# Optimization experiments

Hardware: AMD Instinct MI355X
Metric: run time of the kernel (lower is better)

Reference implementation:

```python
import jax, jax.numpy as jnp
import numpy as np

N = 50000   # nodes
E = 800000  # edges
H = 64      # hidden channels
EPS = 1e-16  # PyG softmax denominator epsilon


def _ptconv(x, pos, src, dst, W_src, W_dst, W_val, W_pos, b_pos):
    """PyG PointTransformerConv: per-edge gather, positional MLP, vector
    attention (segment softmax over edges grouped by dst), scatter-sum.
    edge_index convention: src = j (neighbor), dst = i (center)."""
    a_src = x @ W_src          # [N,H] alpha_j projection
    a_dst = x @ W_dst          # [N,H] alpha_i projection
    v = x @ W_val              # [N,H] values
    # relative positional encoding: pos_nn(pos_i - pos_j), [E,H]
    delta = (pos[dst] - pos[src]) @ W_pos + b_pos
    alpha = a_dst[dst] - a_src[src] + delta           # [E,H]
    # numerically-stable vector softmax over variable-size neighborhoods
    m = jax.lax.stop_gradient(jax.ops.segment_max(alpha, dst, num_segments=N))
    e = jnp.exp(alpha - m[dst])
    s = jax.ops.segment_sum(e, dst, num_segments=N)
    attn = e / (s[dst] + EPS)                         # [E,H]
    return jax.ops.segment_sum(attn * (v[src] + delta), dst, num_segments=N)


def setup_inputs() -> dict:
    key = jax.random.key(0)
    ks = jax.random.split(key, 16)
    x = jax.random.normal(ks[0], (N, 3), dtype=jnp.float32)
    pos = jax.random.normal(ks[1], (N, 3), dtype=jnp.float32)
    edge_index = jax.random.randint(ks[2], (2, E), 0, N)
    batch = jnp.zeros((N,), dtype=jnp.int32)

    def lin(k, i, o):
        return (jax.random.normal(k, (i, o), dtype=jnp.float32)
                * np.float32(1.0 / np.sqrt(i)))

    return {
        "x": x, "pos": pos, "edge_index": edge_index, "batch": batch,
        # conv1 (in=3 -> H)
        "W1_src": lin(ks[3], 3, H), "W1_dst": lin(ks[4], 3, H),
        "W1_val": lin(ks[5], 3, H),
        "W1_pos": lin(ks[6], 3, H), "b1_pos": jnp.zeros((H,), jnp.float32),
        # conv2 (H -> H)
        "W2_src": lin(ks[7], H, H), "W2_dst": lin(ks[8], H, H),
        "W2_val": lin(ks[9], H, H),
        "W2_pos": lin(ks[10], 3, H), "b2_pos": jnp.zeros((H,), jnp.float32),
        # MLP head
        "W_fc1": lin(ks[11], H, H // 2), "b_fc1": jnp.zeros((H // 2,), jnp.float32),
        "W_fc2": lin(ks[12], H // 2, 1), "b_fc2": jnp.zeros((1,), jnp.float32),
    }


def reference(x, pos, edge_index, batch,
              W1_src, W1_dst, W1_val, W1_pos, b1_pos,
              W2_src, W2_dst, W2_val, W2_pos, b2_pos,
              W_fc1, b_fc1, W_fc2, b_fc2):
    src, dst = edge_index[0], edge_index[1]
    h = jax.nn.relu(_ptconv(x, pos, src, dst, W1_src, W1_dst, W1_val, W1_pos, b1_pos))
    h = jax.nn.relu(_ptconv(h, pos, src, dst, W2_src, W2_dst, W2_val, W2_pos, b2_pos))
    h = jax.nn.relu(h @ W_fc1 + b_fc1)
    return h @ W_fc2 + b_fc2  # [N, 1]
```

## Files before the change

### kernel.cpp

```cpp
#include <hip/hip_runtime.h>
#include <hip/hip_fp16.h>
#include <math.h>


#define LOG2E 1.44269504088896340736f

typedef _Float16 hf2 __attribute__((ext_vector_type(2)));
union H2U { __half2 hh; hf2 hf; unsigned u; };
union WPack { uint2 u2; struct { unsigned s, v; } w; };

#if defined(__has_builtin)
#if __has_builtin(__builtin_amdgcn_fdot2)
#define HAVE_FDOT2 1
#endif
#endif

__device__ __forceinline__ float fdot2(hf2 a, hf2 b, float c) {
#ifdef HAVE_FDOT2
    return __builtin_amdgcn_fdot2(a, b, c, false);
#else
    return fmaf((float)a.x, (float)b.x, fmaf((float)a.y, (float)b.y, c));
#endif
}

__global__ void __launch_bounds__(256) hist_proj1_kernel(
        const int* __restrict__ dst, int* __restrict__ count, int* __restrict__ rank,
        const float* __restrict__ x, const float* __restrict__ pos,
        const float* __restrict__ W1_src, const float* __restrict__ W1_val,
        const float* __restrict__ W1_pos,
        __half2* __restrict__ g1, int N, int E) {
    int gtid = blockIdx.x * 256 + threadIdx.x;
    int gsz = gridDim.x * 256;
    for (int e = gtid; e < E; e += gsz)
        rank[e] = atomicAdd(&count[dst[e]], 1);
    for (int t = gtid; t < N * 64; t += gsz) {
        int node = t >> 6, c = t & 63;
        float x0 = x[node * 3 + 0], x1 = x[node * 3 + 1], x2 = x[node * 3 + 2];
        float p0 = pos[node * 3 + 0], p1 = pos[node * 3 + 1], p2 = pos[node * 3 + 2];
        float as = fmaf(x0, W1_src[c], fmaf(x1, W1_src[64 + c], x2 * W1_src[128 + c]));
        float vv = fmaf(x0, W1_val[c], fmaf(x1, W1_val[64 + c], x2 * W1_val[128 + c]));
        float cc = fmaf(p0, W1_pos[c], fmaf(p1, W1_pos[64 + c], p2 * W1_pos[128 + c]));
        g1[t] = __floats2half2_rn((as + cc) * LOG2E, vv - cc);
    }
}

__global__ void __launch_bounds__(256) scan_kernel(
        const int* __restrict__ count, int* __restrict__ offsets, int n, int nsb) {
    __shared__ int red[4];
    __shared__ int wpre[4];
    int tid = threadIdx.x, lane = tid & 63, wid = tid >> 6;
    int lim = blockIdx.x * 1024;
    int s = 0;
    for (int i = tid * 4; i < lim; i += 1024) {
        int4 c = *(const int4*)&count[i];
        s += c.x + c.y + c.z + c.w;
    }
    #pragma unroll
    for (int off = 32; off >= 1; off >>= 1) s += __shfl_down(s, off);
    if (lane == 0) red[wid] = s;
    __syncthreads();
    int base = red[0] + red[1] + red[2] + red[3];

    int b4 = lim + tid * 4;
    int4 c = make_int4(0, 0, 0, 0);
    if (b4 + 3 < n) {
        c = *(const int4*)&count[b4];
    } else {
        if (b4 + 0 < n) c.x = count[b4 + 0];
        if (b4 + 1 < n) c.y = count[b4 + 1];
        if (b4 + 2 < n) c.z = count[b4 + 2];
    }
    int tsum = c.x + c.y + c.z + c.w;
    int inc = tsum;
    #pragma unroll
    for (int off = 1; off < 64; off <<= 1) {
        int t2 = __shfl_up(inc, off);
        if (lane >= off) inc += t2;
    }
    if (lane == 63) wpre[wid] = inc;
    __syncthreads();
    int wbase = 0;
    for (int q = 0; q < wid; ++q) wbase += wpre[q];
    int excl = base + wbase + (inc - tsum);
    if (b4 + 0 < n) offsets[b4 + 0] = excl;
    if (b4 + 1 < n) offsets[b4 + 1] = excl + c.x;
    if (b4 + 2 < n) offsets[b4 + 2] = excl + c.x + c.y;
    if (b4 + 3 < n) offsets[b4 + 3] = excl + c.x + c.y + c.z;
    if ((int)blockIdx.x == nsb - 1 && tid == 0)
        offsets[n] = base + wpre[0] + wpre[1] + wpre[2] + wpre[3];
}

__global__ void __launch_bounds__(256) scatter_kernel(
        const int* __restrict__ src, const int* __restrict__ dst,
        const int* __restrict__ rank, const int* __restrict__ offsets,
        int* __restrict__ sorted_src, int E) {
    int e = blockIdx.x * 256 + threadIdx.x;
    if (e < E) sorted_src[offsets[dst[e]] + rank[e]] = src[e];
}

__device__ __forceinline__ void eacc(float d2, __half2 gh, float& s, float& nvv) {
    float ax = __low2float(gh);
    float vv = __high2float(gh);
    float ev = exp2f(d2 - ax);
    s += ev;
    nvv = fmaf(ev, vv, nvv);
}

__device__ __forceinline__ float edge_node(
        int node, int laneoff,
        const int* __restrict__ offsets, const int* __restrict__ ss,
        const char* __restrict__ gbase, float d2, float dv) {
    int beg = offsets[node], end = offsets[node + 1];
    float s0 = 0.f, n0 = 0.f, s1 = 0.f, n1 = 0.f;
    int e = beg;
    int aligned = min((beg + 3) & ~3, end);
    for (; e < aligned; ++e) {
        int i0 = __builtin_amdgcn_readfirstlane(ss[e]);
        __half2 g0 = *(const __half2*)(gbase + (((size_t)(unsigned)i0) << 8) + laneoff);
        eacc(d2, g0, s0, n0);
    }
    for (; e + 8 <= end; e += 8) {
        int4 ia = *(const int4*)(ss + e);
        int4 ib = *(const int4*)(ss + e + 4);
        int i0 = __builtin_amdgcn_readfirstlane(ia.x);
        int i1 = __builtin_amdgcn_readfirstlane(ia.y);
        int i2 = __builtin_amdgcn_readfirstlane(ia.z);
        int i3 = __builtin_amdgcn_readfirstlane(ia.w);
        int i4 = __builtin_amdgcn_readfirstlane(ib.x);
        int i5 = __builtin_amdgcn_readfirstlane(ib.y);
        int i6 = __builtin_amdgcn_readfirstlane(ib.z);
        int i7 = __builtin_amdgcn_readfirstlane(ib.w);
        __half2 g0 = *(const __half2*)(gbase + (((size_t)(unsigned)i0) << 8) + laneoff);
        __half2 g1 = *(const __half2*)(gbase + (((size_t)(unsigned)i1) << 8) + laneoff);
        __half2 g2 = *(const __half2*)(gbase + (((size_t)(unsigned)i2) << 8) + laneoff);
        __half2 g3 = *(const __half2*)(gbase + (((size_t)(unsigned)i3) << 8) + laneoff);
        __half2 g4 = *(const __half2*)(gbase + (((size_t)(unsigned)i4) << 8) + laneoff);
        __half2 g5 = *(const __half2*)(gbase + (((size_t)(unsigned)i5) << 8) + laneoff);
        __half2 g6 = *(const __half2*)(gbase + (((size_t)(unsigned)i6) << 8) + laneoff);
        __half2 g7 = *(const __half2*)(gbase + (((size_t)(unsigned)i7) << 8) + laneoff);
        eacc(d2, g0, s0, n0);
        eacc(d2, g1, s1, n1);
        eacc(d2, g2, s0, n0);
        eacc(d2, g3, s1, n1);
        eacc(d2, g4, s0, n0);
        eacc(d2, g5, s1, n1);
        eacc(d2, g6, s0, n0);
        eacc(d2, g7, s1, n1);
    }
    for (; e + 4 <= end; e += 4) {
        int4 ia = *(const int4*)(ss + e);
        int i0 = __builtin_amdgcn_readfirstlane(ia.x);
        int i1 = __builtin_amdgcn_readfirstlane(ia.y);
        int i2 = __builtin_amdgcn_readfirstlane(ia.z);
        int i3 = __builtin_amdgcn_readfirstlane(ia.w);
        __half2 g0 = *(const __half2*)(gbase + (((size_t)(unsigned)i0) << 8) + laneoff);
        __half2 g1 = *(const __half2*)(gbase + (((size_t)(unsigned)i1) << 8) + laneoff);
        __half2 g2 = *(const __half2*)(gbase + (((size_t)(unsigned)i2) << 8) + laneoff);
        __half2 g3 = *(const __half2*)(gbase + (((size_t)(unsigned)i3) << 8) + laneoff);
        eacc(d2, g0, s0, n0);
        eacc(d2, g1, s1, n1);
        eacc(d2, g2, s0, n0);
        eacc(d2, g3, s1, n1);
    }
    for (; e < end; ++e) {
        int i0 = __builtin_amdgcn_readfirstlane(ss[e]);
        __half2 g0 = *(const __half2*)(gbase + (((size_t)(unsigned)i0) << 8) + laneoff);
        eacc(d2, g0, s0, n0);
    }
    float s = s0 + s1;
    float num = fmaf(dv, s, n0 + n1);
    return fmaxf(num / (s + 1e-16f), 0.f);
}

__global__ void __launch_bounds__(256, 8) e1p2_kernel(
        const float* __restrict__ pos,
        const int* __restrict__ offsets, const int* __restrict__ sorted_src,
        const __half2* __restrict__ g1,
        const float* __restrict__ W1_pos, const float* __restrict__ b1_pos,
        const float* __restrict__ W2_src, const float* __restrict__ W2_val,
        const float* __restrict__ W2_pos,
        __half2* __restrict__ g2, int N) {
    __shared__ uint2 W4[2048];
    __shared__ __half hsh[4][64];
    int tid = threadIdx.x, lane = tid & 63, wid = tid >> 6;
    for (int idx = tid; idx < 2048; idx += 256) {
        int kk = idx >> 6, c = idx & 63;
        H2U ws, wv;
        ws.hh = __floats2half2_rn(W2_src[(2 * kk) * 64 + c], W2_src[(2 * kk + 1) * 64 + c]);
        wv.hh = __floats2half2_rn(W2_val[(2 * kk) * 64 + c], W2_val[(2 * kk + 1) * 64 + c]);
        W4[idx] = make_uint2(ws.u, wv.u);
    }
    __syncthreads();

    float w1p0 = W1_pos[lane], w1p1 = W1_pos[64 + lane], w1p2 = W1_pos[128 + lane];
    float bp1 = b1_pos[lane];
    float w2p0 = W2_pos[lane], w2p1 = W2_pos[64 + lane], w2p2 = W2_pos[128 + lane];
    int laneoff = lane * 4;
    int nwav = gridDim.x * 4;

    for (int node = blockIdx.x * 4 + wid; node < N; node += nwav) {
        float p0 = pos[node * 3 + 0], p1 = pos[node * 3 + 1], p2 = pos[node * 3 + 2];
        float dpos = fmaf(p0, w1p0, fmaf(p1, w1p1, p2 * w1p2));
        float hval = edge_node(node, laneoff, offsets, sorted_src,
                               (const char*)g1, dpos * LOG2E, dpos + bp1);
        hsh[wid][lane] = __float2half(hval);
        const hf2* h2 = (const hf2*)hsh[wid];
        float as = 0.f, vv = 0.f;
        #pragma unroll 8
        for (int kk = 0; kk < 32; ++kk) {
            hf2 hk = h2[kk];
            WPack wp; wp.u2 = W4[kk * 64 + lane];
            H2U a, b; a.u = wp.w.s; b.u = wp.w.v;
            as = fdot2(hk, a.hf, as);
            vv = fdot2(hk, b.hf, vv);
        }
        float cc = fmaf(p0, w2p0, fmaf(p1, w2p1, p2 * w2p2));
        g2[node * 64 + lane] = __floats2half2_rn((as + cc) * LOG2E, vv - cc);
    }
}

__global__ void __launch_bounds__(256, 8) e2head_kernel(
        const float* __restrict__ pos,
        const int* __restrict__ offsets, const int* __restrict__ sorted_src,
        const __half2* __restrict__ g2,
        const float* __restrict__ W2_pos, const float* __restrict__ b2_pos,
        const float* __restrict__ Wfc1, const float* __restrict__ bfc1,
        const float* __restrict__ Wfc2, const float* __restrict__ bfc2,
        float* __restrict__ out, int N) {
    __shared__ unsigned Wf2[1024];
    __shared__ __half hsh[4][64];
    int tid = threadIdx.x, lane = tid & 63, wid = tid >> 6;
    for (int idx = tid; idx < 1024; idx += 256) {
        int kk = idx >> 5, c = idx & 31;
        H2U w;
        w.hh = __floats2half2_rn(Wfc1[(2 * kk) * 32 + c], Wfc1[(2 * kk + 1) * 32 + c]);
        Wf2[idx] = w.u;
    }
    __syncthreads();

    float wp0 = W2_pos[lane], wp1 = W2_pos[64 + lane], wp2 = W2_pos[128 + lane];
    float bp = b2_pos[lane];
    int c = lane & 31, khb = (lane >> 5) * 16;
    float bfc1c = bfc1[c], wfc2c = Wfc2[c], bias2 = bfc2[0];
    int laneoff = lane * 4;
    int nwav = gridDim.x * 4;

    for (int node = blockIdx.x * 4 + wid; node < N; node += nwav) {
        float p0 = pos[node * 3 + 0], p1 = pos[node * 3 + 1], p2 = pos[node * 3 + 2];
        float dpos = fmaf(p0, wp0, fmaf(p1, wp1, p2 * wp2));
        float hval = edge_node(node, laneoff, offsets, sorted_src,
                               (const char*)g2, dpos * LOG2E, dpos + bp);
        hsh[wid][lane] = __float2half(hval);
        const hf2* h2 = (const hf2*)hsh[wid];
        float t2 = 0.f;
        #pragma unroll 8
        for (int j = 0; j < 16; ++j) {
            hf2 hk = h2[khb + j];
            H2U w; w.u = Wf2[(khb + j) * 32 + c];
            t2 = fdot2(hk, w.hf, t2);
        }
        t2 += __shfl_down(t2, 32);
        t2 = fmaxf(t2 + bfc1c, 0.f) * wfc2c;
        t2 = (lane < 32) ? t2 : 0.f;
        #pragma unroll
        for (int off = 16; off >= 1; off >>= 1) t2 += __shfl_down(t2, off);
        if (lane == 0) out[node] = t2 + bias2;
    }
}

extern "C" void kernel_launch(void* const* d_in, const int* in_sizes, int n_in,
                              void* d_out, int out_size, void* d_ws, size_t ws_size,
                              hipStream_t stream) {
    const float* x   = (const float*)d_in[0];
    const float* pos = (const float*)d_in[1];
    const int* eidx  = (const int*)d_in[2];
    const float* W1_src = (const float*)d_in[4];
    const float* W1_val = (const float*)d_in[6];
    const float* W1_pos = (const float*)d_in[7];
    const float* b1_pos = (const float*)d_in[8];
    const float* W2_src = (const float*)d_in[9];
    const float* W2_val = (const float*)d_in[11];
    const float* W2_pos = (const float*)d_in[12];
    const float* b2_pos = (const float*)d_in[13];
    const float* W_fc1  = (const float*)d_in[14];
    const float* b_fc1  = (const float*)d_in[15];
    const float* W_fc2  = (const float*)d_in[16];
    const float* b_fc2  = (const float*)d_in[17];

    const int N = in_sizes[0] / 3;
    const int E = in_sizes[2] / 2;
    const int* src = eidx;
    const int* dst = eidx + E;
    const int nsb = (N + 1023) / 1024;

    char* w = (char*)d_ws;
    auto carve = [&](size_t bytes) -> void* {
        void* p = (void*)w;
        w += (bytes + 255) & ~size_t(255);
        return p;
    };
    int*     count      = (int*)carve((size_t)N * 4);
    int*     offsets    = (int*)carve((size_t)(N + 1) * 4);
    int*     rank       = (int*)carve((size_t)E * 4);
    int*     sorted_src = (int*)carve((size_t)E * 4);
    __half2* g1         = (__half2*)carve((size_t)N * 64 * 4);
    __half2* g2         = (__half2*)carve((size_t)N * 64 * 4);

    hipMemsetAsync(count, 0, (size_t)N * 4, stream);
    hist_proj1_kernel<<<(N * 64 + 255) / 256, 256, 0, stream>>>(
        dst, count, rank, x, pos, W1_src, W1_val, W1_pos, g1, N, E);
    scan_kernel<<<nsb, 256, 0, stream>>>(count, offsets, N, nsb);
    scatter_kernel<<<(E + 255) / 256, 256, 0, stream>>>(src, dst, rank, offsets,
                                                        sorted_src, E);
    e1p2_kernel<<<2048, 256, 0, stream>>>(
        pos, offsets, sorted_src, g1, W1_pos, b1_pos, W2_src, W2_val, W2_pos, g2, N);
    e2head_kernel<<<2048, 256, 0, stream>>>(
        pos, offsets, sorted_src, g2, W2_pos, b2_pos,
        W_fc1, b_fc1, W_fc2, b_fc2, (float*)d_out, N);
}
```

Before: 246.4 us.

## Factor softmax exponent per source node and gather precomputed fp32 exp payloads

Measured after the change: 269.8 us. 1.09x slower.

```diff
diff --git a/kernel.cpp b/kernel.cpp
--- a/kernel.cpp
+++ b/kernel.cpp
@@ -7,7 +7,6 @@
 
 typedef _Float16 hf2 __attribute__((ext_vector_type(2)));
 union H2U { __half2 hh; hf2 hf; unsigned u; };
-union WPack { uint2 u2; struct { unsigned s, v; } w; };
 
 #if defined(__has_builtin)
 #if __has_builtin(__builtin_amdgcn_fdot2)
@@ -23,24 +22,35 @@
 #endif
 }
 
+__device__ __forceinline__ float2 pack_payload(float a_plus_c, float vv) {
+    float t = fminf(fmaxf(-a_plus_c * LOG2E, -86.6f), 86.6f);
+    float E = exp2f(t);
+    return make_float2(E, E * vv);
+}
+
 __global__ void __launch_bounds__(256) hist_proj1_kernel(
         const int* __restrict__ dst, int* __restrict__ count, int* __restrict__ rank,
         const float* __restrict__ x, const float* __restrict__ pos,
         const float* __restrict__ W1_src, const float* __restrict__ W1_val,
         const float* __restrict__ W1_pos,
-        __half2* __restrict__ g1, int N, int E) {
+        float2* __restrict__ g1, int N, int E) {
     int gtid = blockIdx.x * 256 + threadIdx.x;
     int gsz = gridDim.x * 256;
     for (int e = gtid; e < E; e += gsz)
         rank[e] = atomicAdd(&count[dst[e]], 1);
-    for (int t = gtid; t < N * 64; t += gsz) {
-        int node = t >> 6, c = t & 63;
+
+    int lane = threadIdx.x & 63, wid = threadIdx.x >> 6;
+    float ws0 = W1_src[lane], ws1 = W1_src[64 + lane], ws2 = W1_src[128 + lane];
+    float wv0 = W1_val[lane], wv1 = W1_val[64 + lane], wv2 = W1_val[128 + lane];
+    float wp0 = W1_pos[lane], wp1 = W1_pos[64 + lane], wp2 = W1_pos[128 + lane];
+    int nwav = gridDim.x * 4;
+    for (int node = blockIdx.x * 4 + wid; node < N; node += nwav) {
         float x0 = x[node * 3 + 0], x1 = x[node * 3 + 1], x2 = x[node * 3 + 2];
         float p0 = pos[node * 3 + 0], p1 = pos[node * 3 + 1], p2 = pos[node * 3 + 2];
-        float as = fmaf(x0, W1_src[c], fmaf(x1, W1_src[64 + c], x2 * W1_src[128 + c]));
-        float vv = fmaf(x0, W1_val[c], fmaf(x1, W1_val[64 + c], x2 * W1_val[128 + c]));
-        float cc = fmaf(p0, W1_pos[c], fmaf(p1, W1_pos[64 + c], p2 * W1_pos[128 + c]));
-        g1[t] = __floats2half2_rn((as + cc) * LOG2E, vv - cc);
+        float as = fmaf(x0, ws0, fmaf(x1, ws1, x2 * ws2));
+        float vv = fmaf(x0, wv0, fmaf(x1, wv1, x2 * wv2));
+        float cc = fmaf(p0, wp0, fmaf(p1, wp1, p2 * wp2));
+        g1[node * 64 + lane] = pack_payload(as + cc, vv - cc);
     }
 }
 
@@ -98,26 +108,19 @@
     if (e < E) sorted_src[offsets[dst[e]] + rank[e]] = src[e];
 }
 
-__device__ __forceinline__ void eacc(float d2, __half2 gh, float& s, float& nvv) {
-    float ax = __low2float(gh);
-    float vv = __high2float(gh);
-    float ev = exp2f(d2 - ax);
-    s += ev;
-    nvv = fmaf(ev, vv, nvv);
-}
-
 __device__ __forceinline__ float edge_node(
         int node, int laneoff,
         const int* __restrict__ offsets, const int* __restrict__ ss,
-        const char* __restrict__ gbase, float d2, float dv) {
+        const char* __restrict__ gbase, float dv) {
     int beg = offsets[node], end = offsets[node + 1];
+    if (beg >= end) return 0.f;
     float s0 = 0.f, n0 = 0.f, s1 = 0.f, n1 = 0.f;
     int e = beg;
     int aligned = min((beg + 3) & ~3, end);
     for (; e < aligned; ++e) {
         int i0 = __builtin_amdgcn_readfirstlane(ss[e]);
-        __half2 g0 = *(const __half2*)(gbase + (((size_t)(unsigned)i0) << 8) + laneoff);
-        eacc(d2, g0, s0, n0);
+        float2 g0 = *(const float2*)(gbase + (((size_t)(unsigned)i0) << 9) + laneoff);
+        s0 += g0.x; n0 += g0.y;
     }
     for (; e + 8 <= end; e += 8) {
         int4 ia = *(const int4*)(ss + e);
@@ -130,22 +133,22 @@
         int i5 = __builtin_amdgcn_readfirstlane(ib.y);
         int i6 = __builtin_amdgcn_readfirstlane(ib.z);
         int i7 = __builtin_amdgcn_readfirstlane(ib.w);
-        __half2 g0 = *(const __half2*)(gbase + (((size_t)(unsigned)i0) << 8) + laneoff);
-        __half2 g1 = *(const __half2*)(gbase + (((size_t)(unsigned)i1) << 8) + laneoff);
-        __half2 g2 = *(const __half2*)(gbase + (((size_t)(unsigned)i2) << 8) + laneoff);
-        __half2 g3 = *(const __half2*)(gbase + (((size_t)(unsigned)i3) << 8) + laneoff);
-        __half2 g4 = *(const __half2*)(gbase + (((size_t)(unsigned)i4) << 8) + laneoff);
-        __half2 g5 = *(const __half2*)(gbase + (((size_t)(unsigned)i5) << 8) + laneoff);
-        __half2 g6 = *(const __half2*)(gbase + (((size_t)(unsigned)i6) << 8) + laneoff);
-        __half2 g7 = *(const __half2*)(gbase + (((size_t)(unsigned)i7) << 8) + laneoff);
-        eacc(d2, g0, s0, n0);
-        eacc(d2, g1, s1, n1);
-        eacc(d2, g2, s0, n0);
-        eacc(d2, g3, s1, n1);
-        eacc(d2, g4, s0, n0);
-        eacc(d2, g5, s1, n1);
-        eacc(d2, g6, s0, n0);
-        eacc(d2, g7, s1, n1);
+        float2 g0 = *(const float2*)(gbase + (((size_t)(unsigned)i0) << 9) + laneoff);
+        float2 g1 = *(const float2*)(gbase + (((size_t)(unsigned)i1) << 9) + laneoff);
+        float2 g2 = *(const float2*)(gbase + (((size_t)(unsigned)i2) << 9) + laneoff);
+        float2 g3 = *(const float2*)(gbase + (((size_t)(unsigned)i3) << 9) + laneoff);
+        float2 g4 = *(const float2*)(gbase + (((size_t)(unsigned)i4) << 9) + laneoff);
+        float2 g5 = *(const float2*)(gbase + (((size_t)(unsigned)i5) << 9) + laneoff);
+        float2 g6 = *(const float2*)(gbase + (((size_t)(unsigned)i6) << 9) + laneoff);
+        float2 g7 = *(const float2*)(gbase + (((size_t)(unsigned)i7) << 9) + laneoff);
+        s0 += g0.x; n0 += g0.y;
+        s1 += g1.x; n1 += g1.y;
+        s0 += g2.x; n0 += g2.y;
+        s1 += g3.x; n1 += g3.y;
+        s0 += g4.x; n0 += g4.y;
+        s1 += g5.x; n1 += g5.y;
+        s0 += g6.x; n0 += g6.y;
+        s1 += g7.x; n1 += g7.y;
     }
     for (; e + 4 <= end; e += 4) {
         int4 ia = *(const int4*)(ss + e);
@@ -153,76 +156,82 @@
         int i1 = __builtin_amdgcn_readfirstlane(ia.y);
         int i2 = __builtin_amdgcn_readfirstlane(ia.z);
         int i3 = __builtin_amdgcn_readfirstlane(ia.w);
-        __half2 g0 = *(const __half2*)(gbase + (((size_t)(unsigned)i0) << 8) + laneoff);
-        __half2 g1 = *(const __half2*)(gbase + (((size_t)(unsigned)i1) << 8) + laneoff);
-        __half2 g2 = *(const __half2*)(gbase + (((size_t)(unsigned)i2) << 8) + laneoff);
-        __half2 g3 = *(const __half2*)(gbase + (((size_t)(unsigned)i3) << 8) + laneoff);
-        eacc(d2, g0, s0, n0);
-        eacc(d2, g1, s1, n1);
-        eacc(d2, g2, s0, n0);
-        eacc(d2, g3, s1, n1);
+        float2 g0 = *(const float2*)(gbase + (((size_t)(unsigned)i0) << 9) + laneoff);
+        float2 g1 = *(const float2*)(gbase + (((size_t)(unsigned)i1) << 9) + laneoff);
+        float2 g2 = *(const float2*)(gbase + (((size_t)(unsigned)i2) << 9) + laneoff);
+        float2 g3 = *(const float2*)(gbase + (((size_t)(unsigned)i3) << 9) + laneoff);
+        s0 += g0.x; n0 += g0.y;
+        s1 += g1.x; n1 += g1.y;
+        s0 += g2.x; n0 += g2.y;
+        s1 += g3.x; n1 += g3.y;
     }
     for (; e < end; ++e) {
         int i0 = __builtin_amdgcn_readfirstlane(ss[e]);
-        __half2 g0 = *(const __half2*)(gbase + (((size_t)(unsigned)i0) << 8) + laneoff);
-        eacc(d2, g0, s0, n0);
+        float2 g0 = *(const float2*)(gbase + (((size_t)(unsigned)i0) << 9) + laneoff);
+        s0 += g0.x; n0 += g0.y;
     }
     float s = s0 + s1;
-    float num = fmaf(dv, s, n0 + n1);
-    return fmaxf(num / (s + 1e-16f), 0.f);
+    float r = __builtin_amdgcn_rcpf(s + 1e-37f);
+    return fmaxf(fmaf(n0 + n1, r, dv), 0.f);
 }
 
 __global__ void __launch_bounds__(256, 8) e1p2_kernel(
         const float* __restrict__ pos,
         const int* __restrict__ offsets, const int* __restrict__ sorted_src,
-        const __half2* __restrict__ g1,
+        const float2* __restrict__ g1,
         const float* __restrict__ W1_pos, const float* __restrict__ b1_pos,
         const float* __restrict__ W2_src, const float* __restrict__ W2_val,
         const float* __restrict__ W2_pos,
-        __half2* __restrict__ g2, int N) {
-    __shared__ uint2 W4[2048];
+        float2* __restrict__ g2, int N) {
+    __shared__ uint4 W4q[16 * 64];
     __shared__ __half hsh[4][64];
     int tid = threadIdx.x, lane = tid & 63, wid = tid >> 6;
-    for (int idx = tid; idx < 2048; idx += 256) {
-        int kk = idx >> 6, c = idx & 63;
-        H2U ws, wv;
-        ws.hh = __floats2half2_rn(W2_src[(2 * kk) * 64 + c], W2_src[(2 * kk + 1) * 64 + c]);
-        wv.hh = __floats2half2_rn(W2_val[(2 * kk) * 64 + c], W2_val[(2 * kk + 1) * 64 + c]);
-        W4[idx] = make_uint2(ws.u, wv.u);
+    for (int idx = tid; idx < 1024; idx += 256) {
+        int q = idx >> 6, c = idx & 63, k = 4 * q;
+        H2U s01, s23, v01, v23;
+        s01.hh = __floats2half2_rn(W2_src[k * 64 + c], W2_src[(k + 1) * 64 + c]);
+        s23.hh = __floats2half2_rn(W2_src[(k + 2) * 64 + c], W2_src[(k + 3) * 64 + c]);
+        v01.hh = __floats2half2_rn(W2_val[k * 64 + c], W2_val[(k + 1) * 64 + c]);
+        v23.hh = __floats2half2_rn(W2_val[(k + 2) * 64 + c], W2_val[(k + 3) * 64 + c]);
+        W4q[idx] = make_uint4(s01.u, s23.u, v01.u, v23.u);
     }
     __syncthreads();
 
     float w1p0 = W1_pos[lane], w1p1 = W1_pos[64 + lane], w1p2 = W1_pos[128 + lane];
     float bp1 = b1_pos[lane];
     float w2p0 = W2_pos[lane], w2p1 = W2_pos[64 + lane], w2p2 = W2_pos[128 + lane];
-    int laneoff = lane * 4;
+    int laneoff = lane * 8;
     int nwav = gridDim.x * 4;
 
     for (int node = blockIdx.x * 4 + wid; node < N; node += nwav) {
         float p0 = pos[node * 3 + 0], p1 = pos[node * 3 + 1], p2 = pos[node * 3 + 2];
         float dpos = fmaf(p0, w1p0, fmaf(p1, w1p1, p2 * w1p2));
         float hval = edge_node(node, laneoff, offsets, sorted_src,
-                               (const char*)g1, dpos * LOG2E, dpos + bp1);
+                               (const char*)g1, dpos + bp1);
         hsh[wid][lane] = __float2half(hval);
-        const hf2* h2 = (const hf2*)hsh[wid];
+        const uint2* hq = (const uint2*)hsh[wid];
         float as = 0.f, vv = 0.f;
-        #pragma unroll 8
-        for (int kk = 0; kk < 32; ++kk) {
-            hf2 hk = h2[kk];
-            WPack wp; wp.u2 = W4[kk * 64 + lane];
-            H2U a, b; a.u = wp.w.s; b.u = wp.w.v;
-            as = fdot2(hk, a.hf, as);
-            vv = fdot2(hk, b.hf, vv);
+        #pragma unroll 4
+        for (int q = 0; q < 16; ++q) {
+            uint2 hu = hq[q];
+            H2U h01, h23; h01.u = hu.x; h23.u = hu.y;
+            uint4 wq = W4q[q * 64 + lane];
+            H2U a0, a1, b0, b1;
+            a0.u = wq.x; a1.u = wq.y; b0.u = wq.z; b1.u = wq.w;
+            as = fdot2(h01.hf, a0.hf, as);
+            as = fdot2(h23.hf, a1.hf, as);
+            vv = fdot2(h01.hf, b0.hf, vv);
+            vv = fdot2(h23.hf, b1.hf, vv);
         }
         float cc = fmaf(p0, w2p0, fmaf(p1, w2p1, p2 * w2p2));
-        g2[node * 64 + lane] = __floats2half2_rn((as + cc) * LOG2E, vv - cc);
+        g2[node * 64 + lane] = pack_payload(as + cc, vv - cc);
     }
 }
 
 __global__ void __launch_bounds__(256, 8) e2head_kernel(
         const float* __restrict__ pos,
         const int* __restrict__ offsets, const int* __restrict__ sorted_src,
-        const __half2* __restrict__ g2,
+        const float2* __restrict__ g2,
         const float* __restrict__ W2_pos, const float* __restrict__ b2_pos,
         const float* __restrict__ Wfc1, const float* __restrict__ bfc1,
         const float* __restrict__ Wfc2, const float* __restrict__ bfc2,
@@ -242,14 +251,14 @@
     float bp = b2_pos[lane];
     int c = lane & 31, khb = (lane >> 5) * 16;
     float bfc1c = bfc1[c], wfc2c = Wfc2[c], bias2 = bfc2[0];
-    int laneoff = lane * 4;
+    int laneoff = lane * 8;
     int nwav = gridDim.x * 4;
 
     for (int node = blockIdx.x * 4 + wid; node < N; node += nwav) {
         float p0 = pos[node * 3 + 0], p1 = pos[node * 3 + 1], p2 = pos[node * 3 + 2];
         float dpos = fmaf(p0, wp0, fmaf(p1, wp1, p2 * wp2));
         float hval = edge_node(node, laneoff, offsets, sorted_src,
-                               (const char*)g2, dpos * LOG2E, dpos + bp);
+                               (const char*)g2, dpos + bp);
         hsh[wid][lane] = __float2half(hval);
         const hf2* h2 = (const hf2*)hsh[wid];
         float t2 = 0.f;
@@ -299,15 +308,15 @@
         w += (bytes + 255) & ~size_t(255);
         return p;
     };
-    int*     count      = (int*)carve((size_t)N * 4);
-    int*     offsets    = (int*)carve((size_t)(N + 1) * 4);
-    int*     rank       = (int*)carve((size_t)E * 4);
-    int*     sorted_src = (int*)carve((size_t)E * 4);
-    __half2* g1         = (__half2*)carve((size_t)N * 64 * 4);
-    __half2* g2         = (__half2*)carve((size_t)N * 64 * 4);
+    int*    count      = (int*)carve((size_t)N * 4);
+    int*    offsets    = (int*)carve((size_t)(N + 1) * 4);
+    int*    rank       = (int*)carve((size_t)E * 4);
+    int*    sorted_src = (int*)carve((size_t)E * 4);
+    float2* g1         = (float2*)carve((size_t)N * 64 * 8);
+    float2* g2         = (float2*)carve((size_t)N * 64 * 8);
 
     hipMemsetAsync(count, 0, (size_t)N * 4, stream);
-    hist_proj1_kernel<<<(N * 64 + 255) / 256, 256, 0, stream>>>(
+    hist_proj1_kernel<<<2048, 256, 0, stream>>>(
         dst, count, rank, x, pos, W1_src, W1_val, W1_pos, g1, N, E);
     scan_kernel<<<nsb, 256, 0, stream>>>(count, offsets, N, nsb);
     scatter_kernel<<<(E + 255) / 256, 256, 0, stream>>>(src, dst, rank, offsets,
```
